# Kernel optimization log

Measured on AMD Instinct MI355X. Metric: run time of the kernel, lower is better.

## Reference

```python
import jax, jax.numpy as jnp
import numpy as np

INPUT_DIM = 512


def setup_inputs() -> dict:
    key = jax.random.key(0)
    ks = jax.random.split(key, 9)
    B = 262144
    d = INPUT_DIM
    inp = {
        "combined": jax.random.normal(ks[0], (B, 2 * d), dtype=jnp.float32),
        "W_in": jax.random.normal(ks[1], (d, 128), dtype=jnp.float32) / np.sqrt(d),
        "b_in": jax.random.normal(ks[2], (128,), dtype=jnp.float32) * 0.01,
        "W1": jax.random.normal(ks[3], (128, 128), dtype=jnp.float32) / np.sqrt(128.0),
        "b1": jax.random.normal(ks[4], (128,), dtype=jnp.float32) * 0.01,
        "W2": jax.random.normal(ks[5], (128, 64), dtype=jnp.float32) / np.sqrt(128.0),
        "b2": jax.random.normal(ks[6], (64,), dtype=jnp.float32) * 0.01,
        "W_out": jax.random.normal(ks[7], (128, 1), dtype=jnp.float32) / np.sqrt(128.0),
        "b_out": jax.random.normal(ks[8], (1,), dtype=jnp.float32) * 0.01,
    }
    return inp


def reference(combined, W_in, b_in, W1, b1, W2, b2, W_out, b_out):
    d = INPUT_DIM
    # Build per-sample 2-node graphs: nodes = (subj, obj). Shape [B, 2, d]
    x = jnp.stack([combined[:, :d], combined[:, d:]], axis=1)
    h = jax.nn.relu(x @ W_in + b_in)  # [B, 2, 128]

    # GCNConv on the 2-node graph (edges 0<->1 + default self-loops):
    # deg(i)=2, edge norm = 1/sqrt(2)*1/sqrt(2)=0.5, so both nodes get
    # 0.5*(h0 W + h1 W) + b == mean over nodes, transformed.
    def gcn(h, W, b):
        m = jnp.mean(h, axis=1, keepdims=True) @ W + b  # [B, 1, out]
        return jnp.broadcast_to(m, (h.shape[0], 2, W.shape[1]))

    h = jax.nn.relu(gcn(h, W1, b1))  # [B, 2, 128]
    h = jax.nn.relu(gcn(h, W2, b2))  # [B, 2, 64]

    combined_nodes = jnp.concatenate([h[:, 0], h[:, 1]], axis=-1)  # [B, 128]
    score = combined_nodes @ W_out + b_out  # [B, 1]
    return jax.nn.sigmoid(score)
```

## Files before the change

### kernel.cpp

```cpp
#include <hip/hip_runtime.h>
#include <hip/hip_bf16.h>
#include <cstdint>
#include <cstddef>


#define NROWS   524288
#define NSAMP   262144

typedef __attribute__((ext_vector_type(8))) short  bf16x8;
typedef __attribute__((ext_vector_type(4))) float  f32x4;
typedef __attribute__((ext_vector_type(2))) unsigned int u32x2;

#define LGKM0() asm volatile("s_waitcnt lgkmcnt(0)" ::: "memory")
#define VMW0()  asm volatile("s_waitcnt vmcnt(0)" ::: "memory")
#define BAR()   __builtin_amdgcn_s_barrier()

__device__ __forceinline__ unsigned short f2bf(float f) {
    unsigned u = __float_as_uint(f);
    u += 0x7fffu + ((u >> 16) & 1u);
    return (unsigned short)(u >> 16);
}

__device__ __forceinline__ f32x4 mfma16(bf16x8 a, bf16x8 b, f32x4 c) {
    return __builtin_amdgcn_mfma_f32_16x16x32_bf16(a, b, c, 0, 0, 0);
}

#define WS_M     0
#define WS_WIN   67108864
#define WS_W1    67239936
#define WS_W2    67272704
#define WS_WEFF  67289088

__global__ void prep_kernel(const float* __restrict__ W_in,
                            const float* __restrict__ W1,
                            const float* __restrict__ W2,
                            const float* __restrict__ W_out,
                            unsigned short* __restrict__ fWin,
                            unsigned short* __restrict__ fW1,
                            unsigned short* __restrict__ fW2,
                            float* __restrict__ weff) {
    int tid = blockIdx.x * 256 + threadIdx.x;
    if (tid < 65536) {
        int e = tid;
        int j = e & 7, l = (e >> 3) & 63, rest = e >> 9;
        int n = rest & 7, kt = rest >> 3;
        int k = kt * 32 + ((l >> 4) << 3) + j;
        int col = n * 16 + (l & 15);
        fWin[e] = f2bf(W_in[k * 128 + col]);
    } else if (tid < 65536 + 16384) {
        int e = tid - 65536;
        int j = e & 7, l = (e >> 3) & 63, rest = e >> 9;
        int n = rest & 7, kt = rest >> 3;
        int k = kt * 32 + ((l >> 4) << 3) + j;
        int col = n * 16 + (l & 15);
        fW1[e] = f2bf(W1[k * 128 + col]);
    } else if (tid < 65536 + 16384 + 8192) {
        int e = tid - 65536 - 16384;
        int j = e & 7, l = (e >> 3) & 63, rest = e >> 9;
        int n = rest & 3, kt = rest >> 2;
        int k = kt * 32 + ((l >> 4) << 3) + j;
        int col = n * 16 + (l & 15);
        fW2[e] = f2bf(W2[k * 64 + col]);
    } else if (tid < 65536 + 16384 + 8192 + 64) {
        int c = tid - (65536 + 16384 + 8192);
        weff[c] = W_out[c] + W_out[64 + c];
    }
}

__global__ void __launch_bounds__(512) __attribute__((amdgpu_waves_per_eu(2, 2)))
kA(const float* __restrict__ A,
   const unsigned short* __restrict__ fWin,
   const float* __restrict__ b_in,
   unsigned short* __restrict__ Mf) {
    __shared__ __align__(16) char lds[73728];
    char* buf0 = lds;
    char* buf1 = lds + 32768;
    char* bnc0 = lds + 65536;
    char* bnc1 = lds + 69632;

    const int tid = threadIdx.x, w = tid >> 6, l = tid & 63;
    const int lr = l & 15, lg = l >> 4;

    bf16x8 wfr[16];
    #pragma unroll
    for (int kt = 0; kt < 16; ++kt)
        wfr[kt] = *(const bf16x8*)&fWin[((kt * 8 + w) * 64 + l) * 8];
    const float bb = b_in[w * 16 + lr];

    const float* Ablk = A + (size_t)blockIdx.x * 2048 * 512;
    const int lrow  = tid >> 7;
    const int lcol2 = ((tid * 4) & 511) * 2;

    f32x4 stg[8];
    f32x4 acc0, acc1;

    #define ISSUE(t) { const float* p = Ablk + (size_t)(t) * 16384 + tid * 4; \
        _Pragma("unroll") for (int r = 0; r < 8; ++r) stg[r] = *(const f32x4*)(p + r * 2048); }
    #define CVTWR(buf) { _Pragma("unroll") \
        for (int r = 0; r < 8; ++r) { \
            const int row = r * 4 + lrow; \
            char* d = (buf) + row * 1024 + (lcol2 ^ ((row & 7) << 4)); \
            unsigned pa, pb; \
            asm("v_cvt_pk_bf16_f32 %0, %1, %2" : "=v"(pa) : "v"(stg[r][0]), "v"(stg[r][1])); \
            asm("v_cvt_pk_bf16_f32 %0, %1, %2" : "=v"(pb) : "v"(stg[r][2]), "v"(stg[r][3])); \
            u32x2 pk; pk[0] = pa; pk[1] = pb; \
            *(u32x2*)d = pk; } }

    ISSUE(0); VMW0(); CVTWR(buf0); LGKM0(); BAR();

    for (int t = 0; t < 64; ++t) {
        char* cur = (t & 1) ? buf1 : buf0;
        char* nxt = (t & 1) ? buf0 : buf1;
        char* bc  = (t & 1) ? bnc1 : bnc0;
        if (t < 63) ISSUE(t + 1);

        acc0 = (f32x4){0.f, 0.f, 0.f, 0.f};
        acc1 = (f32x4){0.f, 0.f, 0.f, 0.f};
        #pragma unroll
        for (int kg = 0; kg < 16; ++kg) {
            const int co = kg * 64 + lg * 16;
            const int sw0 = co ^ ((lr & 7) << 4);
            bf16x8 a0v = *(const bf16x8*)(cur + lr * 1024 + sw0);
            bf16x8 a1v = *(const bf16x8*)(cur + (16 + lr) * 1024 + sw0);
            acc0 = mfma16(a0v, wfr[kg], acc0);
            acc1 = mfma16(a1v, wfr[kg], acc1);
        }

        {
            const int c2 = (w * 16 + lr) * 2;
            float m0 = 0.5f * (fmaxf(acc0[0] + bb, 0.f) + fmaxf(acc0[1] + bb, 0.f));
            float m1 = 0.5f * (fmaxf(acc0[2] + bb, 0.f) + fmaxf(acc0[3] + bb, 0.f));
            int s0 = 2 * lg, s1 = s0 + 1;
            *(unsigned short*)(bc + s0 * 256 + (c2 ^ ((s0 & 7) << 4))) = f2bf(m0);
            *(unsigned short*)(bc + s1 * 256 + (c2 ^ ((s1 & 7) << 4))) = f2bf(m1);
            float m2 = 0.5f * (fmaxf(acc1[0] + bb, 0.f) + fmaxf(acc1[1] + bb, 0.f));
            float m3 = 0.5f * (fmaxf(acc1[2] + bb, 0.f) + fmaxf(acc1[3] + bb, 0.f));
            int s2 = 8 + 2 * lg, s3 = s2 + 1;
            *(unsigned short*)(bc + s2 * 256 + (c2 ^ ((s2 & 7) << 4))) = f2bf(m2);
            *(unsigned short*)(bc + s3 * 256 + (c2 ^ ((s3 & 7) << 4))) = f2bf(m3);
        }

        if (t < 63) { VMW0(); CVTWR(nxt); }
        LGKM0(); BAR();

        if (w < 4) {
            int roff = lr * 256 + ((w * 64 + lg * 16) ^ ((lr & 7) << 4));
            bf16x8 v = *(const bf16x8*)(bc + roff);
            size_t F = (size_t)blockIdx.x * 64 + (size_t)t;
            *(bf16x8*)&Mf[F * 2048 + (size_t)w * 512 + (size_t)l * 8] = v;
        }
    }
    #undef ISSUE
    #undef CVTWR
}

__global__ void __launch_bounds__(256, 2)
kB(const unsigned short* __restrict__ Mf,
   const unsigned short* __restrict__ fW1,
   const unsigned short* __restrict__ fW2,
   const float* __restrict__ weff,
   const float* __restrict__ b1,
   const float* __restrict__ b2,
   const float* __restrict__ b_out,
   float* __restrict__ out) {
    __shared__ unsigned short lw1[16384];
    __shared__ unsigned short lw2[8192];
    __shared__ unsigned short bounce[4][2048];
    {
        int tid = threadIdx.x;
        const f32x4* s1 = (const f32x4*)fW1;
        f32x4* d1 = (f32x4*)lw1;
        #pragma unroll
        for (int i = 0; i < 8; ++i) d1[i * 256 + tid] = s1[i * 256 + tid];
        const f32x4* s2 = (const f32x4*)fW2;
        f32x4* d2 = (f32x4*)lw2;
        #pragma unroll
        for (int i = 0; i < 4; ++i) d2[i * 256 + tid] = s2[i * 256 + tid];
    }
    __syncthreads();
    const int w = threadIdx.x >> 6, l = threadIdx.x & 63;
    const int lr = l & 15, lg = l >> 4;
    float b1v[8], b2v[4], wev[4];
    #pragma unroll
    for (int n = 0; n < 8; ++n) b1v[n] = b1[n * 16 + lr];
    #pragma unroll
    for (int n = 0; n < 4; ++n) { b2v[n] = b2[n * 16 + lr]; wev[n] = weff[n * 16 + lr]; }
    const float bo = b_out[0];

    for (int t = blockIdx.x; t < NSAMP / 64; t += 512) {
        const int s0 = t * 64 + w * 16;
        const size_t F = (size_t)t * 4 + (size_t)w;
        f32x4 acc1[8];
        #pragma unroll
        for (int n = 0; n < 8; ++n) acc1[n] = (f32x4){0.f, 0.f, 0.f, 0.f};
        #pragma unroll
        for (int ks = 0; ks < 4; ++ks) {
            bf16x8 af = *(const bf16x8*)&Mf[F * 2048 + ks * 512 + l * 8];
            #pragma unroll
            for (int n = 0; n < 8; ++n) {
                bf16x8 bf = *(const bf16x8*)&lw1[((ks * 8 + n) * 64 + l) * 8];
                acc1[n] = __builtin_amdgcn_mfma_f32_16x16x32_bf16(af, bf, acc1[n], 0, 0, 0);
            }
        }
        #pragma unroll
        for (int n = 0; n < 8; ++n) {
            #pragma unroll
            for (int rr = 0; rr < 4; ++rr) {
                float g = fmaxf(acc1[n][rr] + b1v[n], 0.f);
                int row = lg * 4 + rr, col = n * 16 + lr;
                int boff = row * 256 + ((col * 2) ^ ((row & 7) << 4));
                bounce[w][boff >> 1] = f2bf(g);
            }
        }
        f32x4 acc2[4];
        #pragma unroll
        for (int n = 0; n < 4; ++n) acc2[n] = (f32x4){0.f, 0.f, 0.f, 0.f};
        #pragma unroll
        for (int ks = 0; ks < 4; ++ks) {
            int roff = lr * 256 + ((ks * 64 + lg * 16) ^ ((lr & 7) << 4));
            bf16x8 af2 = *(const bf16x8*)((const char*)&bounce[w][0] + roff);
            #pragma unroll
            for (int n = 0; n < 4; ++n) {
                bf16x8 bf = *(const bf16x8*)&lw2[((ks * 4 + n) * 64 + l) * 8];
                acc2[n] = __builtin_amdgcn_mfma_f32_16x16x32_bf16(af2, bf, acc2[n], 0, 0, 0);
            }
        }
        float p0 = 0.f, p1 = 0.f, p2 = 0.f, p3 = 0.f;
        #pragma unroll
        for (int n = 0; n < 4; ++n) {
            p0 += fmaxf(acc2[n][0] + b2v[n], 0.f) * wev[n];
            p1 += fmaxf(acc2[n][1] + b2v[n], 0.f) * wev[n];
            p2 += fmaxf(acc2[n][2] + b2v[n], 0.f) * wev[n];
            p3 += fmaxf(acc2[n][3] + b2v[n], 0.f) * wev[n];
        }
        #pragma unroll
        for (int m = 1; m < 16; m <<= 1) {
            p0 += __shfl_xor(p0, m);
            p1 += __shfl_xor(p1, m);
            p2 += __shfl_xor(p2, m);
            p3 += __shfl_xor(p3, m);
        }
        float s0f = 1.f / (1.f + expf(-(p0 + bo)));
        float s1f = 1.f / (1.f + expf(-(p1 + bo)));
        float s2f = 1.f / (1.f + expf(-(p2 + bo)));
        float s3f = 1.f / (1.f + expf(-(p3 + bo)));
        if (lr < 4) {
            float v = (lr == 0) ? s0f : (lr == 1) ? s1f : (lr == 2) ? s2f : s3f;
            out[s0 + lg * 4 + lr] = v;
        }
    }
}

extern "C" void kernel_launch(void* const* d_in, const int* in_sizes, int n_in,
                              void* d_out, int out_size, void* d_ws, size_t ws_size,
                              hipStream_t stream) {
    const float* combined = (const float*)d_in[0];
    const float* W_in  = (const float*)d_in[1];
    const float* b_in  = (const float*)d_in[2];
    const float* W1    = (const float*)d_in[3];
    const float* b1    = (const float*)d_in[4];
    const float* W2    = (const float*)d_in[5];
    const float* b2    = (const float*)d_in[6];
    const float* W_out = (const float*)d_in[7];
    const float* b_out = (const float*)d_in[8];
    float* out = (float*)d_out;

    char* ws = (char*)d_ws;
    unsigned short* Mf   = (unsigned short*)(ws + WS_M);
    unsigned short* fWin = (unsigned short*)(ws + WS_WIN);
    unsigned short* fW1  = (unsigned short*)(ws + WS_W1);
    unsigned short* fW2  = (unsigned short*)(ws + WS_W2);
    float* weff          = (float*)(ws + WS_WEFF);

    prep_kernel<<<(65536 + 16384 + 8192 + 64 + 255) / 256, 256, 0, stream>>>(
        W_in, W1, W2, W_out, fWin, fW1, fW2, weff);
    kA<<<256, 512, 0, stream>>>(combined, fWin, b_in, Mf);
    kB<<<512, 256, 0, stream>>>(Mf, fW1, fW2, weff, b1, b2, b_out, out);
}
```

Measured before the change: 307.6 us.

## Load fp32 input tiles directly to LDS and convert to bf16 at MFMA time

```diff
diff --git a/kernel.cpp b/kernel.cpp
--- a/kernel.cpp
+++ b/kernel.cpp
@@ -9,16 +9,29 @@
 
 typedef __attribute__((ext_vector_type(8))) short  bf16x8;
 typedef __attribute__((ext_vector_type(4))) float  f32x4;
-typedef __attribute__((ext_vector_type(2))) unsigned int u32x2;
 
 #define LGKM0() asm volatile("s_waitcnt lgkmcnt(0)" ::: "memory")
 #define VMW0()  asm volatile("s_waitcnt vmcnt(0)" ::: "memory")
 #define BAR()   __builtin_amdgcn_s_barrier()
+
+#define GLOAD_LDS(gsrc, ldst) \
+    __builtin_amdgcn_global_load_lds( \
+        (const __attribute__((address_space(1))) void*)(gsrc), \
+        (__attribute__((address_space(3))) void*)(ldst), 16, 0, 0)
 
 __device__ __forceinline__ unsigned short f2bf(float f) {
     unsigned u = __float_as_uint(f);
     u += 0x7fffu + ((u >> 16) & 1u);
     return (unsigned short)(u >> 16);
+}
+
+__device__ __forceinline__ bf16x8 cvt8(f32x4 lo, f32x4 hi) {
+    union { unsigned u[4]; bf16x8 v; } r;
+    asm("v_cvt_pk_bf16_f32 %0, %1, %2" : "=v"(r.u[0]) : "v"(lo[0]), "v"(lo[1]));
+    asm("v_cvt_pk_bf16_f32 %0, %1, %2" : "=v"(r.u[1]) : "v"(lo[2]), "v"(lo[3]));
+    asm("v_cvt_pk_bf16_f32 %0, %1, %2" : "=v"(r.u[2]) : "v"(hi[0]), "v"(hi[1]));
+    asm("v_cvt_pk_bf16_f32 %0, %1, %2" : "=v"(r.u[3]) : "v"(hi[2]), "v"(hi[3]));
+    return r.v;
 }
 
 __device__ __forceinline__ f32x4 mfma16(bf16x8 a, bf16x8 b, f32x4 c) {
@@ -72,11 +85,11 @@
    const unsigned short* __restrict__ fWin,
    const float* __restrict__ b_in,
    unsigned short* __restrict__ Mf) {
-    __shared__ __align__(16) char lds[73728];
+    __shared__ __align__(16) char lds[139264];
     char* buf0 = lds;
-    char* buf1 = lds + 32768;
-    char* bnc0 = lds + 65536;
-    char* bnc1 = lds + 69632;
+    char* buf1 = lds + 65536;
+    char* bnc0 = lds + 131072;
+    char* bnc1 = lds + 135168;
 
     const int tid = threadIdx.x, w = tid >> 6, l = tid & 63;
     const int lr = l & 15, lg = l >> 4;
@@ -87,43 +100,45 @@
         wfr[kt] = *(const bf16x8*)&fWin[((kt * 8 + w) * 64 + l) * 8];
     const float bb = b_in[w * 16 + lr];
 
-    const float* Ablk = A + (size_t)blockIdx.x * 2048 * 512;
-    const int lrow  = tid >> 7;
-    const int lcol2 = ((tid * 4) & 511) * 2;
-
-    f32x4 stg[8];
-    f32x4 acc0, acc1;
-
-    #define ISSUE(t) { const float* p = Ablk + (size_t)(t) * 16384 + tid * 4; \
-        _Pragma("unroll") for (int r = 0; r < 8; ++r) stg[r] = *(const f32x4*)(p + r * 2048); }
-    #define CVTWR(buf) { _Pragma("unroll") \
-        for (int r = 0; r < 8; ++r) { \
-            const int row = r * 4 + lrow; \
-            char* d = (buf) + row * 1024 + (lcol2 ^ ((row & 7) << 4)); \
-            unsigned pa, pb; \
-            asm("v_cvt_pk_bf16_f32 %0, %1, %2" : "=v"(pa) : "v"(stg[r][0]), "v"(stg[r][1])); \
-            asm("v_cvt_pk_bf16_f32 %0, %1, %2" : "=v"(pb) : "v"(stg[r][2]), "v"(stg[r][3])); \
-            u32x2 pk; pk[0] = pa; pk[1] = pb; \
-            *(u32x2*)d = pk; } }
-
-    ISSUE(0); VMW0(); CVTWR(buf0); LGKM0(); BAR();
+    const char* Ablk = (const char*)(A + (size_t)blockIdx.x * 2048 * 512);
+
+    int loff[8];
+    #pragma unroll
+    for (int r = 0; r < 8; ++r) {
+        int row = w * 4 + (r >> 1);
+        int u = (r & 1) * 64 + l;
+        loff[r] = row * 2048 + ((u ^ (row & 7)) * 16);
+    }
+
+    const int e1 = (((lg * 2)     ^ (lr & 7)) * 16);
+    const int e2 = (((lg * 2 + 1) ^ (lr & 7)) * 16);
+    const int rb0 = lr * 2048, rb1 = (16 + lr) * 2048;
+
+    #define ISSUE(t, buf) { \
+        const char* gb = Ablk + (size_t)(t) * 65536; \
+        char* db = (buf) + w * 8192; \
+        _Pragma("unroll") \
+        for (int r = 0; r < 8; ++r) \
+            GLOAD_LDS(gb + loff[r], db + r * 1024); }
+
+    ISSUE(0, buf0); VMW0(); BAR();
 
     for (int t = 0; t < 64; ++t) {
         char* cur = (t & 1) ? buf1 : buf0;
         char* nxt = (t & 1) ? buf0 : buf1;
         char* bc  = (t & 1) ? bnc1 : bnc0;
-        if (t < 63) ISSUE(t + 1);
-
-        acc0 = (f32x4){0.f, 0.f, 0.f, 0.f};
-        acc1 = (f32x4){0.f, 0.f, 0.f, 0.f};
+        if (t < 63) ISSUE(t + 1, nxt);
+
+        f32x4 acc0 = (f32x4){0.f, 0.f, 0.f, 0.f};
+        f32x4 acc1 = (f32x4){0.f, 0.f, 0.f, 0.f};
         #pragma unroll
         for (int kg = 0; kg < 16; ++kg) {
-            const int co = kg * 64 + lg * 16;
-            const int sw0 = co ^ ((lr & 7) << 4);
-            bf16x8 a0v = *(const bf16x8*)(cur + lr * 1024 + sw0);
-            bf16x8 a1v = *(const bf16x8*)(cur + (16 + lr) * 1024 + sw0);
-            acc0 = mfma16(a0v, wfr[kg], acc0);
-            acc1 = mfma16(a1v, wfr[kg], acc1);
+            f32x4 p0a = *(const f32x4*)(cur + rb0 + kg * 128 + e1);
+            f32x4 p0b = *(const f32x4*)(cur + rb0 + kg * 128 + e2);
+            f32x4 p1a = *(const f32x4*)(cur + rb1 + kg * 128 + e1);
+            f32x4 p1b = *(const f32x4*)(cur + rb1 + kg * 128 + e2);
+            acc0 = mfma16(cvt8(p0a, p0b), wfr[kg], acc0);
+            acc1 = mfma16(cvt8(p1a, p1b), wfr[kg], acc1);
         }
 
         {
@@ -140,8 +155,9 @@
             *(unsigned short*)(bc + s3 * 256 + (c2 ^ ((s3 & 7) << 4))) = f2bf(m3);
         }
 
-        if (t < 63) { VMW0(); CVTWR(nxt); }
-        LGKM0(); BAR();
+        LGKM0();
+        if (t < 63) VMW0();
+        BAR();
 
         if (w < 4) {
             int roff = lr * 256 + ((w * 64 + lg * 16) ^ ((lr & 7) << 4));
@@ -151,7 +167,6 @@
         }
     }
     #undef ISSUE
-    #undef CVTWR
 }
 
 __global__ void __launch_bounds__(256, 2)
```

Measured after the change: 291.0 us. 5.4% less time.
